# Kernel optimization log

Measured on AMD Instinct MI355X. Metric: run time of the kernel, lower is better.

## Reference

```python
import jax, jax.numpy as jnp
import numpy as np

B, D, N, M = 64, 128, 400, 50
H, KD = 8, 16
NCONV, K, PAD = 4, 7, 3
MAXTS = 10000.0


def _pe(l):
    # PositionEncoding: freqs/phases interleave sin/cos as sin(pos*f + phase)
    i = np.arange(D)
    freqs = MAXTS ** np.where(i % 2 == 0, -i / D, -(i - 1) / D)
    phases = np.where(i % 2 == 0, 0.0, np.pi / 2)
    pos = np.arange(l)
    return jnp.asarray(np.sin(pos[None, :] * freqs[:, None] + phases[:, None]).astype(np.float32))  # [D, l]


def _ln(x, g, b, eps=1e-6):
    # LayerNorm1d over channel dim of [B, D, L]; torch .std() is unbiased (ddof=1), divides by (std+eps)
    mu = x.mean(axis=1, keepdims=True)
    sd = x.std(axis=1, keepdims=True, ddof=1)
    return g[None, :, None] * (x - mu) / (sd + eps) + b[None, :, None]


def _attn(xT, mask, Wq, bq, Wk, bk, Wv, bv, Wo, bo):
    # xT: [B, L, D]; per-head linears vectorized over the head axis
    q = jnp.einsum('bld,hdk->bhlk', xT, Wq) + bq[None, :, None, :]
    k = jnp.einsum('bld,hdk->bhlk', xT, Wk) + bk[None, :, None, :]
    v = jnp.einsum('bld,hdk->bhlk', xT, Wv) + bv[None, :, None, :]
    sc = jnp.einsum('bhik,bhjk->bhij', q, k) / np.sqrt(KD)
    sc = sc - 1e30 * (1.0 - mask[:, None, None, :])  # mask over key positions
    a = jax.nn.softmax(sc, axis=-1)
    o = jnp.einsum('bhij,bhjk->bhik', a, v)
    o = o.transpose(0, 2, 1, 3).reshape(xT.shape[0], xT.shape[1], H * KD)
    return o @ Wo + bo


def _fwd(context_emb, question_emb, c_mask, q_mask, ln_g, ln_b, dw_w, dw_b, pw_w, pw_b,
         Wq, bq, Wk, bk, Wv, bv, Wo, bo, Wfc, bfc, cq_wc, cq_wq, cq_wm, cq_b):
    def block(x, mask):
        out = x + _pe(x.shape[2])[None]
        for i in range(NCONV):  # fixed small layer loop
            res = out
            h = _ln(out, ln_g, ln_b)
            h = jax.lax.conv_general_dilated(h, dw_w[i], (1,), [(PAD, PAD)],
                                             feature_group_count=D,
                                             dimension_numbers=('NCH', 'OIH', 'NCH')) + dw_b[i][None, :, None]
            h = jnp.einsum('bdl,ed->bel', h, pw_w[i]) + pw_b[i][None, :, None]
            out = jax.nn.relu(h) + res  # eval-mode layer_dropout = inputs + residual
        res = out
        h = _ln(out, ln_g, ln_b)
        h = _attn(h.transpose(0, 2, 1), mask, Wq, bq, Wk, bk, Wv, bv, Wo, bo)
        out = h.transpose(0, 2, 1) + res
        res = out
        h = _ln(out, ln_g, ln_b)
        h = jnp.einsum('bdl,ed->bel', h, Wfc) + bfc[None, :, None]
        return h + res

    C = block(context_emb, c_mask)
    Q = block(question_emb, q_mask)
    C2 = C.transpose(0, 2, 1)  # [B, N, D]
    Q2 = Q.transpose(0, 2, 1)  # [B, M, D]
    # Biaffine similarity W0([Q; C; Q*C]) decomposed (same math, no [B,N*M,3D] materialization)
    S = (C2 @ cq_wc)[:, :, None] + (Q2 @ cq_wq)[:, None, :] \
        + jnp.einsum('bnd,bmd->bnm', C2 * cq_wm, Q2) + cq_b[0]
    S_r = jax.nn.softmax(S - 1e30 * (1.0 - q_mask[:, None, :]), axis=2)
    S_c = jax.nn.softmax(S - 1e30 * (1.0 - c_mask[:, :, None]), axis=1)
    A = S_r @ Q2                                    # context-to-query [B, N, D]
    Bt = jnp.einsum('bnm,bkm->bnk', S_r, S_c) @ C2  # query-to-context (DCN style) [B, N, D]
    return jnp.concatenate([C2, A, C2 * A, C2 * Bt], axis=-1)  # [B, N, 4D]


def setup_inputs() -> dict:
    key = jax.random.key(0)
    ks = jax.random.split(key, 16)
    s = 1.0 / np.sqrt(D)
    return dict(
        context_emb=jax.random.normal(ks[0], (B, D, N), jnp.float32),
        question_emb=jax.random.normal(ks[1], (B, D, M), jnp.float32),
        c_mask=jnp.ones((B, N), jnp.float32),
        q_mask=jnp.ones((B, M), jnp.float32),
        ln_g=jnp.ones((D,), jnp.float32),
        ln_b=jnp.zeros((D,), jnp.float32),
        dw_w=jax.random.normal(ks[2], (NCONV, D, 1, K), jnp.float32) / np.sqrt(K),
        dw_b=jnp.zeros((NCONV, D), jnp.float32),
        pw_w=jax.random.normal(ks[3], (NCONV, D, D), jnp.float32) * s,
        pw_b=jnp.zeros((NCONV, D), jnp.float32),
        Wq=jax.random.normal(ks[4], (H, D, KD), jnp.float32) * s,
        bq=jnp.zeros((H, KD), jnp.float32),
        Wk=jax.random.normal(ks[5], (H, D, KD), jnp.float32) * s,
        bk=jnp.zeros((H, KD), jnp.float32),
        Wv=jax.random.normal(ks[6], (H, D, KD), jnp.float32) * s,
        bv=jnp.zeros((H, KD), jnp.float32),
        Wo=jax.random.normal(ks[7], (H * KD, D), jnp.float32) * s,
        bo=jnp.zeros((D,), jnp.float32),
        Wfc=jax.random.normal(ks[8], (D, D), jnp.float32) * s,
        bfc=jnp.zeros((D,), jnp.float32),
        cq_wc=jax.random.normal(ks[9], (D,), jnp.float32) * s,
        cq_wq=jax.random.normal(ks[10], (D,), jnp.float32) * s,
        cq_wm=jax.random.normal(ks[11], (D,), jnp.float32) * s,
        cq_b=jnp.zeros((1,), jnp.float32),
    )


def reference(context_emb, question_emb, c_mask, q_mask, ln_g, ln_b, dw_w, dw_b, pw_w, pw_b,
              Wq, bq, Wk, bk, Wv, bv, Wo, bo, Wfc, bfc, cq_wc, cq_wq, cq_wm, cq_b):
    return _fwd(context_emb, question_emb, c_mask, q_mask, ln_g, ln_b, dw_w, dw_b, pw_w, pw_b,
                Wq, bq, Wk, bk, Wv, bv, Wo, bo, Wfc, bfc, cq_wc, cq_wq, cq_wm, cq_b)
```

## Files before the change

### kernel.cpp

```cpp
#include <hip/hip_runtime.h>
#include <math.h>

#define BB 64
#define DD 128
#define NN 400
#define MM 50
#define HH 8
#define KDIM 16
#define NC 4
#define KW 7

#define SZ_C (BB * DD * NN)
#define SZ_Q (BB * DD * MM)
#define SSTAT (BB * NN + BB * MM)

__global__ void k_transposeW(const float* __restrict__ pw_w, const float* __restrict__ Wo,
                             const float* __restrict__ Wfc, const float* __restrict__ Wq,
                             const float* __restrict__ Wk, const float* __restrict__ Wv,
                             float* __restrict__ Wcan) {
  int idx = blockIdx.x * 256 + threadIdx.x;
  if (idx >= 9 * 16384) return;
  int m = idx >> 14;
  int r = idx & 16383;
  int d = r >> 7, e = r & 127;
  float v;
  if (m < 4) v = pw_w[m * 16384 + e * 128 + d];
  else if (m == 4) v = Wo[d * 128 + e];
  else if (m == 5) v = Wfc[e * 128 + d];
  else {
    const float* W = (m == 6) ? Wq : (m == 7) ? Wk : Wv;
    v = W[((e >> 4) * 128 + d) * 16 + (e & 15)];
  }
  Wcan[idx] = v;
}

__global__ void k_pestats(const float* __restrict__ xC, const float* __restrict__ xQ,
                          float* __restrict__ yC, float* __restrict__ yQ,
                          float* __restrict__ mu, float* __restrict__ inv) {
  int blk = blockIdx.x;
  const float* x; float* y; int L, l0, b, soff;
  if (blk < 448) { b = blk / 7; l0 = (blk % 7) * 64; x = xC; y = yC; L = NN; soff = 0; }
  else { b = blk - 448; l0 = 0; x = xQ; y = yQ; L = MM; soff = BB * NN; }
  int tid = threadIdx.x;
  int ll = tid & 63;
  int dq = tid >> 6;
  int l = l0 + ll;
  __shared__ float s_sum[4][64], s_sq[4][64];
  float sum = 0.f, sq = 0.f;
  if (l < L) {
    const float* px = x + (size_t)b * DD * L + l;
    float* py = y + (size_t)b * DD * L + l;
    for (int d = dq * 32; d < dq * 32 + 32; ++d) {
      int de = d & ~1;
      float freq = __expf((float)de * (-9.210340371976184f / 128.0f));
      float ph = (d & 1) ? 1.5707963267948966f : 0.0f;
      float v = px[(size_t)d * L] + sinf((float)l * freq + ph);
      py[(size_t)d * L] = v;
      sum += v; sq += v * v;
    }
  }
  s_sum[dq][ll] = sum; s_sq[dq][ll] = sq;
  __syncthreads();
  if (dq == 0 && l < L) {
    float ts = s_sum[0][ll] + s_sum[1][ll] + s_sum[2][ll] + s_sum[3][ll];
    float tq = s_sq[0][ll] + s_sq[1][ll] + s_sq[2][ll] + s_sq[3][ll];
    float m = ts * (1.0f / 128.0f);
    float var = (tq - 128.0f * m * m) * (1.0f / 127.0f);
    float sd = sqrtf(fmaxf(var, 0.f));
    mu[soff + b * L + l] = m;
    inv[soff + b * L + l] = 1.0f / (sd + 1e-6f);
  }
}

__global__ __launch_bounds__(256, 2) void k_convgemm(
    const float* __restrict__ xC, const float* __restrict__ xQ,
    float* __restrict__ outC, float* __restrict__ outQ,
    const float* __restrict__ Wc, const float* __restrict__ pwb,
    const float* __restrict__ dww, const float* __restrict__ dwb,
    const float* __restrict__ muI, const float* __restrict__ invI,
    float* __restrict__ muO, float* __restrict__ invO,
    const float* __restrict__ g, const float* __restrict__ beta) {
  int blk = blockIdx.x;
  int b = blk >> 3, tile = blk & 7;
  const float* x; float* out; int L, l0, soff;
  if (tile < 7) { x = xC; out = outC; L = NN; l0 = tile * 64; soff = 0; }
  else { x = xQ; out = outQ; L = MM; l0 = 0; soff = BB * NN; }
  __shared__ float Wl[32 * 128];
  __shared__ float Xl[32 * 64];
  __shared__ float Sm[70], Si[70];
  int tid = threadIdx.x;
  const float* xb = x + (size_t)b * DD * L;
  for (int t = tid; t < 70; t += 256) {
    int gl = l0 + t - 3;
    bool ok = (gl >= 0 && gl < L);
    Sm[t] = ok ? muI[soff + b * L + gl] : 0.f;
    Si[t] = ok ? invI[soff + b * L + gl] : 0.f;
  }
  float acc[8][4];
  #pragma unroll
  for (int i = 0; i < 8; ++i)
    #pragma unroll
    for (int j = 0; j < 4; ++j) acc[i][j] = 0.f;
  __syncthreads();
  for (int kc = 0; kc < 4; ++kc) {
    int d0 = kc * 32;
    #pragma unroll
    for (int i = 0; i < 4; ++i) {
      int idx = i * 256 + tid;
      ((float4*)Wl)[idx] = ((const float4*)Wc)[(size_t)d0 * 32 + idx];
    }
    #pragma unroll
    for (int r = 0; r < 2; ++r) {
      int k = r * 16 + (tid >> 4);
      int d = d0 + k;
      int c0 = (tid & 15) * 4;
      const float* xrow = xb + (size_t)d * L;
      float gd = g[d], bd = beta[d];
      float wv[7];
      #pragma unroll
      for (int u = 0; u < 7; ++u) wv[u] = dww[d * 7 + u];
      float dbv = dwb[d];
      float xw[10];
      int gbase = l0 + c0 - 3;
      if (gbase >= 1 && gbase + 11 <= L && (((unsigned)(d * L + gbase - 1)) & 3u) == 0u) {
        const float4* p = (const float4*)&xrow[gbase - 1];
        float4 A = p[0], Bv = p[1], Cv = p[2];
        float xr[12] = {A.x, A.y, A.z, A.w, Bv.x, Bv.y, Bv.z, Bv.w, Cv.x, Cv.y, Cv.z, Cv.w};
        #pragma unroll
        for (int s = 0; s < 10; ++s)
          xw[s] = gd * (xr[s + 1] - Sm[c0 + s]) * Si[c0 + s] + bd;
      } else {
        #pragma unroll
        for (int s = 0; s < 10; ++s) {
          int gl = gbase + s;
          float v = 0.f;
          if (gl >= 0 && gl < L)
            v = gd * (xrow[gl] - Sm[c0 + s]) * Si[c0 + s] + bd;
          xw[s] = v;
        }
      }
      float4 o;
      o.x = dbv; o.y = dbv; o.z = dbv; o.w = dbv;
      #pragma unroll
      for (int u = 0; u < 7; ++u) {
        o.x += wv[u] * xw[u];
        o.y += wv[u] * xw[u + 1];
        o.z += wv[u] * xw[u + 2];
        o.w += wv[u] * xw[u + 3];
      }
      *(float4*)&Xl[k * 64 + c0] = o;
    }
    __syncthreads();
    int e0 = (tid >> 4) * 8, cq = (tid & 15) * 4;
    for (int k = 0; k < 32; ++k) {
      const float4* wp = (const float4*)&Wl[k * 128 + e0];
      float4 w0 = wp[0], w1 = wp[1];
      float4 xv = *(const float4*)&Xl[k * 64 + cq];
      float we[8] = {w0.x, w0.y, w0.z, w0.w, w1.x, w1.y, w1.z, w1.w};
      float xe[4] = {xv.x, xv.y, xv.z, xv.w};
      #pragma unroll
      for (int i = 0; i < 8; ++i)
        #pragma unroll
        for (int j = 0; j < 4; ++j) acc[i][j] += we[i] * xe[j];
    }
    __syncthreads();
  }
  int e0 = (tid >> 4) * 8, cq = (tid & 15) * 4;
  float ssum[4], ssq[4];
  #pragma unroll
  for (int j = 0; j < 4; ++j) { ssum[j] = 0.f; ssq[j] = 0.f; }
  #pragma unroll
  for (int i = 0; i < 8; ++i) {
    float bi = pwb[e0 + i];
    float* po = out + ((size_t)b * DD + e0 + i) * L;
    const float* pr = xb + (size_t)(e0 + i) * L;
    #pragma unroll
    for (int j = 0; j < 4; ++j) {
      int l = l0 + cq + j;
      if (l < L) {
        float v = fmaxf(acc[i][j] + bi, 0.f) + pr[l];
        po[l] = v;
        ssum[j] += v; ssq[j] += v * v;
      }
    }
  }
  int grp = tid >> 4;
  #pragma unroll
  for (int j = 0; j < 4; ++j) {
    Xl[grp * 64 + cq + j] = ssum[j];
    Wl[grp * 64 + cq + j] = ssq[j];
  }
  __syncthreads();
  if (tid < 64) {
    int l = l0 + tid;
    if (l < L) {
      float ts = 0.f, tq = 0.f;
      #pragma unroll
      for (int gg = 0; gg < 16; ++gg) { ts += Xl[gg * 64 + tid]; tq += Wl[gg * 64 + tid]; }
      float m = ts * (1.0f / 128.0f);
      float var = (tq - 128.0f * m * m) * (1.0f / 127.0f);
      float sd = sqrtf(fmaxf(var, 0.f));
      muO[soff + b * L + l] = m;
      invO[soff + b * L + l] = 1.0f / (sd + 1e-6f);
    }
  }
}

template <int LNF, int ACT, int STATS>
__global__ __launch_bounds__(256) void k_gemm64(
    const float* __restrict__ xC, const float* __restrict__ xQ,
    float* __restrict__ outC, float* __restrict__ outQ,
    const float* __restrict__ Wc, const float* __restrict__ bias,
    const float* __restrict__ mu, const float* __restrict__ inv,
    float* __restrict__ muO, float* __restrict__ invO,
    const float* __restrict__ g, const float* __restrict__ beta) {
  int blk = blockIdx.x;
  int b = blk >> 3, tile = blk & 7;
  const float* x; float* out; int L, l0, soff;
  if (tile < 7) { x = xC; out = outC; L = NN; l0 = tile * 64; soff = 0; }
  else { x = xQ; out = outQ; L = MM; l0 = 0; soff = BB * NN; }
  __shared__ float Wl[32 * 128];
  __shared__ float Xl[32 * 64];
  int tid = threadIdx.x;
  float acc[8][4];
  #pragma unroll
  for (int i = 0; i < 8; ++i)
    #pragma unroll
    for (int j = 0; j < 4; ++j) acc[i][j] = 0.f;
  const float* xb = x + (size_t)b * DD * L;
  const float* pmu = mu + soff + b * L;
  const float* pin = inv + soff + b * L;
  for (int kc = 0; kc < 4; ++kc) {
    int d0 = kc * 32;
    #pragma unroll
    for (int i = 0; i < 4; ++i) {
      int idx = i * 256 + tid;
      ((float4*)Wl)[idx] = ((const float4*)Wc)[(size_t)d0 * 32 + idx];
    }
    #pragma unroll
    for (int t = 0; t < 8; ++t) {
      int idx = t * 256 + tid;
      int k = idx >> 6, l = idx & 63;
      float v = 0.f;
      int gl = l0 + l;
      if (gl < L) {
        v = xb[(size_t)(d0 + k) * L + gl];
        if (LNF) v = g[d0 + k] * (v - pmu[gl]) * pin[gl] + beta[d0 + k];
      }
      Xl[idx] = v;
    }
    __syncthreads();
    int e0 = (tid >> 4) * 8, cq = (tid & 15) * 4;
    for (int k = 0; k < 32; ++k) {
      const float4* wp = (const float4*)&Wl[k * 128 + e0];
      float4 w0 = wp[0], w1 = wp[1];
      float4 xv = *(const float4*)&Xl[k * 64 + cq];
      float we[8] = {w0.x, w0.y, w0.z, w0.w, w1.x, w1.y, w1.z, w1.w};
      float xe[4] = {xv.x, xv.y, xv.z, xv.w};
      #pragma unroll
      for (int i = 0; i < 8; ++i)
        #pragma unroll
        for (int j = 0; j < 4; ++j) acc[i][j] += we[i] * xe[j];
    }
    __syncthreads();
  }
  int e0 = (tid >> 4) * 8, cq = (tid & 15) * 4;
  float ssum[4], ssq[4];
  #pragma unroll
  for (int j = 0; j < 4; ++j) { ssum[j] = 0.f; ssq[j] = 0.f; }
  #pragma unroll
  for (int i = 0; i < 8; ++i) {
    float bi = bias[e0 + i];
    float* po = out + ((size_t)b * DD + e0 + i) * L;
    #pragma unroll
    for (int j = 0; j < 4; ++j) {
      int l = l0 + cq + j;
      if (l < L) {
        float v = acc[i][j] + bi;
        if (ACT != 0) v += po[l];
        po[l] = v;
        if (STATS) { ssum[j] += v; ssq[j] += v * v; }
      }
    }
  }
  if (STATS) {
    int grp = tid >> 4;
    #pragma unroll
    for (int j = 0; j < 4; ++j) {
      Xl[grp * 64 + cq + j] = ssum[j];
      Wl[grp * 64 + cq + j] = ssq[j];
    }
    __syncthreads();
    if (tid < 64) {
      int l = l0 + tid;
      if (l < L) {
        float ts = 0.f, tq = 0.f;
        #pragma unroll
        for (int gg = 0; gg < 16; ++gg) { ts += Xl[gg * 64 + tid]; tq += Wl[gg * 64 + tid]; }
        float m = ts * (1.0f / 128.0f);
        float var = (tq - 128.0f * m * m) * (1.0f / 127.0f);
        float sd = sqrtf(fmaxf(var, 0.f));
        muO[soff + b * L + l] = m;
        invO[soff + b * L + l] = 1.0f / (sd + 1e-6f);
      }
    }
  }
}

__global__ __launch_bounds__(256) void k_gemm_qkv(
    const float* __restrict__ xC, const float* __restrict__ xQ,
    float* __restrict__ o1C, float* __restrict__ o1Q,
    float* __restrict__ o2C, float* __restrict__ o2Q,
    float* __restrict__ o3C, float* __restrict__ o3Q,
    const float* __restrict__ Wcan,
    const float* __restrict__ bq, const float* __restrict__ bk, const float* __restrict__ bv,
    const float* __restrict__ mu, const float* __restrict__ inv,
    const float* __restrict__ g, const float* __restrict__ beta) {
  int blk0 = blockIdx.x;
  int grp = blk0 >> 9;
  int blk = blk0 & 511;
  const float* Wc = Wcan + (size_t)(6 + grp) * 16384;
  const float* bias = (grp == 0) ? bq : (grp == 1) ? bk : bv;
  float* oC = (grp == 0) ? o1C : (grp == 1) ? o2C : o3C;
  float* oQ = (grp == 0) ? o1Q : (grp == 1) ? o2Q : o3Q;
  int b = blk >> 3, tile = blk & 7;
  const float* x; float* out; int L, l0, soff;
  if (tile < 7) { x = xC; out = oC; L = NN; l0 = tile * 64; soff = 0; }
  else { x = xQ; out = oQ; L = MM; l0 = 0; soff = BB * NN; }
  __shared__ float Wl[32 * 128];
  __shared__ float Xl[32 * 64];
  int tid = threadIdx.x;
  float acc[8][4];
  #pragma unroll
  for (int i = 0; i < 8; ++i)
    #pragma unroll
    for (int j = 0; j < 4; ++j) acc[i][j] = 0.f;
  const float* xb = x + (size_t)b * DD * L;
  const float* pmu = mu + soff + b * L;
  const float* pin = inv + soff + b * L;
  for (int kc = 0; kc < 4; ++kc) {
    int d0 = kc * 32;
    #pragma unroll
    for (int i = 0; i < 4; ++i) {
      int idx = i * 256 + tid;
      ((float4*)Wl)[idx] = ((const float4*)Wc)[(size_t)d0 * 32 + idx];
    }
    #pragma unroll
    for (int t = 0; t < 8; ++t) {
      int idx = t * 256 + tid;
      int k = idx >> 6, l = idx & 63;
      float v = 0.f;
      int gl = l0 + l;
      if (gl < L) {
        v = xb[(size_t)(d0 + k) * L + gl];
        v = g[d0 + k] * (v - pmu[gl]) * pin[gl] + beta[d0 + k];
      }
      Xl[idx] = v;
    }
    __syncthreads();
    int e0 = (tid >> 4) * 8, cq = (tid & 15) * 4;
    for (int k = 0; k < 32; ++k) {
      const float4* wp = (const float4*)&Wl[k * 128 + e0];
      float4 w0 = wp[0], w1 = wp[1];
      float4 xv = *(const float4*)&Xl[k * 64 + cq];
      float we[8] = {w0.x, w0.y, w0.z, w0.w, w1.x, w1.y, w1.z, w1.w};
      float xe[4] = {xv.x, xv.y, xv.z, xv.w};
      #pragma unroll
      for (int i = 0; i < 8; ++i)
        #pragma unroll
        for (int j = 0; j < 4; ++j) acc[i][j] += we[i] * xe[j];
    }
    __syncthreads();
  }
  int e0 = (tid >> 4) * 8, cq = (tid & 15) * 4;
  #pragma unroll
  for (int i = 0; i < 8; ++i) {
    float bi = bias[e0 + i];
    float* po = out + ((size_t)b * DD + e0 + i) * L;
    #pragma unroll
    for (int j = 0; j < 4; ++j) {
      int l = l0 + cq + j;
      if (l < L) po[l] = acc[i][j] + bi;
    }
  }
}

__global__ __launch_bounds__(256) void k_attn2(
    const float* __restrict__ qC, const float* __restrict__ kC, const float* __restrict__ vC,
    const float* __restrict__ qQ, const float* __restrict__ kQ, const float* __restrict__ vQ,
    const float* __restrict__ cmask, const float* __restrict__ qmask,
    float* __restrict__ oC, float* __restrict__ oQ) {
  int blk = blockIdx.x;
  const float *qp, *kp, *vp, *mk; float* op; int L, b, h, q0, qcnt;
  if (blk < 1024) {
    b = blk >> 4; h = (blk >> 1) & 7; int half = blk & 1;
    qp = qC; kp = kC; vp = vC; mk = cmask; op = oC; L = NN;
    q0 = half * 256; qcnt = half ? (NN - 256) : 256;
  } else {
    int bb = blk - 1024; b = bb >> 3; h = bb & 7;
    qp = qQ; kp = kQ; vp = vQ; mk = qmask; op = oQ; L = MM;
    q0 = 0; qcnt = MM;
  }
  __shared__ float Kl[NN * KDIM];
  __shared__ float Vl[NN * KDIM];
  __shared__ float Ml[NN];
  int tid = threadIdx.x;
  size_t base = ((size_t)b * DD + h * KDIM) * L;
  int KP = (L + 7) & ~7;
  for (int idx = tid; idx < KDIM * L; idx += 256) {
    int t = idx / L, j = idx - t * L;
    Kl[j * KDIM + t] = kp[base + (size_t)t * L + j];
    Vl[j * KDIM + t] = vp[base + (size_t)t * L + j];
  }
  for (int idx = tid; idx < (KP - L) * KDIM; idx += 256) {
    int j = L + (idx >> 4), t = idx & 15;
    Kl[j * KDIM + t] = 0.f; Vl[j * KDIM + t] = 0.f;
  }
  for (int j = tid; j < KP; j += 256)
    Ml[j] = (j < L) ? -1e30f * (1.0f - mk[b * L + j]) : -1e30f;
  __syncthreads();
  if (tid >= qcnt) return;

  int i = q0 + tid;
  float q[KDIM];
  #pragma unroll
  for (int t = 0; t < KDIM; ++t) q[t] = qp[base + (size_t)t * L + i] * 0.25f;
  float m = -1e30f, ls = 0.f;
  float acc[KDIM];
  #pragma unroll
  for (int t = 0; t < KDIM; ++t) acc[t] = 0.f;
  for (int j0 = 0; j0 < KP; j0 += 8) {
    const float4* mp = (const float4*)&Ml[j0];
    float4 ma0 = mp[0], ma1 = mp[1];
    float mav[8] = {ma0.x, ma0.y, ma0.z, ma0.w, ma1.x, ma1.y, ma1.z, ma1.w};
    float s[8];
    #pragma unroll
    for (int jj = 0; jj < 8; ++jj) {
      const float4* kf = (const float4*)&Kl[(j0 + jj) * KDIM];
      float4 k0 = kf[0], k1 = kf[1], k2 = kf[2], k3 = kf[3];
      float da = q[0] * k0.x + q[1] * k0.y + q[2] * k0.z + q[3] * k0.w
               + q[4] * k1.x + q[5] * k1.y + q[6] * k1.z + q[7] * k1.w;
      float db = q[8] * k2.x + q[9] * k2.y + q[10] * k2.z + q[11] * k2.w
               + q[12] * k3.x + q[13] * k3.y + q[14] * k3.z + q[15] * k3.w;
      s[jj] = da + db + mav[jj];
    }
    float cm = s[0];
    #pragma unroll
    for (int jj = 1; jj < 8; ++jj) cm = fmaxf(cm, s[jj]);
    if (cm > m) {
      float sc = __expf(m - cm);
      ls *= sc;
      #pragma unroll
      for (int t = 0; t < KDIM; ++t) acc[t] *= sc;
      m = cm;
    }
    #pragma unroll
    for (int jj = 0; jj < 8; ++jj) {
      float p = __expf(s[jj] - m);
      ls += p;
      const float4* vf = (const float4*)&Vl[(j0 + jj) * KDIM];
      float4 v0 = vf[0], v1 = vf[1], v2 = vf[2], v3 = vf[3];
      acc[0] += p * v0.x;  acc[1] += p * v0.y;  acc[2] += p * v0.z;  acc[3] += p * v0.w;
      acc[4] += p * v1.x;  acc[5] += p * v1.y;  acc[6] += p * v1.z;  acc[7] += p * v1.w;
      acc[8] += p * v2.x;  acc[9] += p * v2.y;  acc[10] += p * v2.z; acc[11] += p * v2.w;
      acc[12] += p * v3.x; acc[13] += p * v3.y; acc[14] += p * v3.z; acc[15] += p * v3.w;
    }
  }
  float invl = 1.0f / ls;
  #pragma unroll
  for (int t = 0; t < KDIM; ++t)
    op[base + (size_t)t * L + i] = acc[t] * invl;
}

__global__ void k_prep(const float* __restrict__ Cb, const float* __restrict__ Qb,
                       float* __restrict__ C2, float* __restrict__ Q2,
                       const float* __restrict__ wc, const float* __restrict__ wq,
                       float* __restrict__ cd, float* __restrict__ qd) {
  int blk = blockIdx.x, tid = threadIdx.x;
  if (blk < 3840) {
    const float* X; float* Y; int L, rem;
    if (blk < 3328) { X = Cb; Y = C2; L = NN; rem = blk; }
    else { X = Qb; Y = Q2; L = MM; rem = blk - 3328; }
    int ntl = (L + 31) / 32;
    int b = rem / (4 * ntl);
    int r2 = rem % (4 * ntl);
    int d0 = (r2 / ntl) * 32;
    int l0 = (r2 % ntl) * 32;
    __shared__ float T[32][33];
    int c = tid & 31, r8 = tid >> 5;
    const float* xb = X + (size_t)b * DD * L;
    #pragma unroll
    for (int k = 0; k < 4; ++k) {
      int r = r8 + k * 8;
      int l = l0 + c;
      T[r][c] = (l < L) ? xb[(size_t)(d0 + r) * L + l] : 0.f;
    }
    __syncthreads();
    float* yb = Y + (size_t)b * L * DD;
    #pragma unroll
    for (int k = 0; k < 4; ++k) {
      int rr = r8 + k * 8;
      int l = l0 + rr;
      if (l < L) yb[(size_t)l * DD + d0 + c] = T[c][rr];
    }
  } else if (blk < 3940) {
    int idx = (blk - 3840) * 256 + tid;
    if (idx < BB * NN) {
      int l = idx % NN, b = idx / NN;
      const float* px = Cb + (size_t)b * DD * NN + l;
      float acc = 0.f;
      for (int d = 0; d < DD; ++d) acc += px[(size_t)d * NN] * wc[d];
      cd[idx] = acc;
    }
  } else {
    int idx = (blk - 3940) * 256 + tid;
    if (idx < BB * MM) {
      int l = idx % MM, b = idx / MM;
      const float* px = Qb + (size_t)b * DD * MM + l;
      float acc = 0.f;
      for (int d = 0; d < DD; ++d) acc += px[(size_t)d * MM] * wq[d];
      qd[idx] = acc;
    }
  }
}

__global__ void k_S(const float* __restrict__ C2, const float* __restrict__ Q2,
                    const float* __restrict__ cd, const float* __restrict__ qd,
                    const float* __restrict__ wm, const float* __restrict__ bias,
                    float* __restrict__ S) {
  int idx = blockIdx.x * 256 + threadIdx.x;
  if (idx >= BB * NN * MM) return;
  int mcol = idx % MM;
  int n = (idx / MM) % NN;
  int b = idx / (MM * NN);
  const float4* pc = (const float4*)(C2 + ((size_t)b * NN + n) * DD);
  const float4* pq = (const float4*)(Q2 + ((size_t)b * MM + mcol) * DD);
  const float4* pw = (const float4*)wm;
  float a0 = 0.f, a1 = 0.f;
  #pragma unroll 4
  for (int d4 = 0; d4 < 32; d4 += 2) {
    float4 c0 = pc[d4], w0 = pw[d4], q0 = pq[d4];
    float4 c1 = pc[d4 + 1], w1 = pw[d4 + 1], q1 = pq[d4 + 1];
    a0 += (c0.x * w0.x) * q0.x + (c0.y * w0.y) * q0.y + (c0.z * w0.z) * q0.z + (c0.w * w0.w) * q0.w;
    a1 += (c1.x * w1.x) * q1.x + (c1.y * w1.y) * q1.y + (c1.z * w1.z) * q1.z + (c1.w * w1.w) * q1.w;
  }
  S[idx] = a0 + a1 + cd[b * NN + n] + qd[b * MM + mcol] + bias[0];
}

__global__ void k_smax(const float* __restrict__ S, float* __restrict__ Sr,
                       float* __restrict__ Sc, const float* __restrict__ cmask,
                       const float* __restrict__ qmask) {
  int blk = blockIdx.x;
  int tid = threadIdx.x;
  if (blk < BB * MM) {
    int b = blk / MM;
    int mcol = blk % MM;
    float vals[7];
    float mx = -1e30f;
    #pragma unroll
    for (int c = 0; c < 7; ++c) {
      int n = tid + c * 64;
      float s = -1e30f;
      if (n < NN)
        s = S[((size_t)b * NN + n) * MM + mcol] - 1e30f * (1.0f - cmask[b * NN + n]);
      vals[c] = s;
      mx = fmaxf(mx, s);
    }
    #pragma unroll
    for (int off = 1; off < 64; off <<= 1) mx = fmaxf(mx, __shfl_xor(mx, off));
    float sum = 0.f;
    #pragma unroll
    for (int c = 0; c < 7; ++c) { vals[c] = __expf(vals[c] - mx); sum += vals[c]; }
    #pragma unroll
    for (int off = 1; off < 64; off <<= 1) sum += __shfl_xor(sum, off);
    float inv = 1.0f / sum;
    #pragma unroll
    for (int c = 0; c < 7; ++c) {
      int n = tid + c * 64;
      if (n < NN) Sc[((size_t)b * NN + n) * MM + mcol] = vals[c] * inv;
    }
  } else {
    int bn = blk - BB * MM;
    int b = bn / NN;
    float s = -1e30f;
    if (tid < MM)
      s = S[(size_t)bn * MM + tid] - 1e30f * (1.0f - qmask[b * MM + tid]);
    float mx = s;
    #pragma unroll
    for (int off = 1; off < 64; off <<= 1) mx = fmaxf(mx, __shfl_xor(mx, off));
    float e = (tid < MM) ? __expf(s - mx) : 0.f;
    float sum = e;
    #pragma unroll
    for (int off = 1; off < 64; off <<= 1) sum += __shfl_xor(sum, off);
    if (tid < MM) Sr[(size_t)bn * MM + tid] = e / sum;
  }
}

__global__ void k_U(const float* __restrict__ Sc, const float* __restrict__ C2,
                    float* __restrict__ U) {
  int idx = blockIdx.x * 256 + threadIdx.x;
  if (idx >= BB * MM * 32) return;
  int d4 = idx & 31;
  int rest = idx >> 5;
  int mcol = rest % MM;
  int b = rest / MM;
  const float* psc = Sc + (size_t)b * NN * MM + mcol;
  const float4* pc2 = (const float4*)(C2 + (size_t)b * NN * DD) + d4;
  float4 acc = {0.f, 0.f, 0.f, 0.f};
  #pragma unroll 4
  for (int kk = 0; kk < NN; ++kk) {
    float s = psc[(size_t)kk * MM];
    float4 c = pc2[(size_t)kk * 32];
    acc.x += s * c.x; acc.y += s * c.y; acc.z += s * c.z; acc.w += s * c.w;
  }
  ((float4*)U)[idx] = acc;
}

__global__ __launch_bounds__(256) void k_ABtF(
    const float* __restrict__ Sr, const float* __restrict__ Q2,
    const float* __restrict__ Uu, const float* __restrict__ C2,
    float* __restrict__ out) {
  int blk = blockIdx.x;
  int b = blk / 7, nt = blk % 7;
  int n0 = nt * 64;
  int nv = NN - n0; if (nv > 64) nv = 64;
  __shared__ float Ql[MM * 128];
  __shared__ float Ul[MM * 128];
  __shared__ float Sl[64 * MM];
  int tid = threadIdx.x;
  const float4* q4 = (const float4*)(Q2 + (size_t)b * MM * DD);
  const float4* u4 = (const float4*)(Uu + (size_t)b * MM * DD);
  for (int i = tid; i < MM * 32; i += 256) {
    ((float4*)Ql)[i] = q4[i];
    ((float4*)Ul)[i] = u4[i];
  }
  for (int i = tid; i < 64 * MM; i += 256) {
    int n = i / MM;
    Sl[i] = (n < nv) ? Sr[((size_t)b * NN + n0 + n) * MM + (i - n * MM)] : 0.f;
  }
  __syncthreads();
  int n = tid >> 2;
  if (n >= nv) return;
  int d04 = (tid & 3) * 8;
  float4 accA[8], accB[8];
  #pragma unroll
  for (int r = 0; r < 8; ++r) {
    accA[r] = {0.f, 0.f, 0.f, 0.f};
    accB[r] = {0.f, 0.f, 0.f, 0.f};
  }
  const float* sp = &Sl[n * MM];
  for (int m = 0; m < MM; ++m) {
    float s = sp[m];
    const float4* qp = (const float4*)&Ql[m * 128] + d04;
    const float4* up = (const float4*)&Ul[m * 128] + d04;
    #pragma unroll
    for (int r = 0; r < 8; ++r) {
      float4 q = qp[r], u = up[r];
      accA[r].x += s * q.x; accA[r].y += s * q.y; accA[r].z += s * q.z; accA[r].w += s * q.w;
      accB[r].x += s * u.x; accB[r].y += s * u.y; accB[r].z += s * u.z; accB[r].w += s * u.w;
    }
  }
  int gn = n0 + n;
  const float4* c4 = (const float4*)(C2 + ((size_t)b * NN + gn) * DD) + d04;
  float4* po = (float4*)(out + (size_t)(b * NN + gn) * 512);
  #pragma unroll
  for (int r = 0; r < 8; ++r) {
    float4 c = c4[r];
    float4 a = accA[r], bt = accB[r];
    po[d04 + r] = c;
    po[32 + d04 + r] = a;
    float4 ca = {c.x * a.x, c.y * a.y, c.z * a.z, c.w * a.w};
    po[64 + d04 + r] = ca;
    float4 cb = {c.x * bt.x, c.y * bt.y, c.z * bt.z, c.w * bt.w};
    po[96 + d04 + r] = cb;
  }
}

extern "C" void kernel_launch(void* const* d_in, const int* in_sizes, int n_in,
                              void* d_out, int out_size, void* d_ws, size_t ws_size,
                              hipStream_t stream) {
  (void)in_sizes; (void)n_in; (void)out_size; (void)ws_size;
  const float* ctx   = (const float*)d_in[0];
  const float* que   = (const float*)d_in[1];
  const float* cmask = (const float*)d_in[2];
  const float* qmask = (const float*)d_in[3];
  const float* ln_g  = (const float*)d_in[4];
  const float* ln_b  = (const float*)d_in[5];
  const float* dw_w  = (const float*)d_in[6];
  const float* dw_b  = (const float*)d_in[7];
  const float* pw_w  = (const float*)d_in[8];
  const float* pw_b  = (const float*)d_in[9];
  const float* Wq    = (const float*)d_in[10];
  const float* bq    = (const float*)d_in[11];
  const float* Wk    = (const float*)d_in[12];
  const float* bk    = (const float*)d_in[13];
  const float* Wv    = (const float*)d_in[14];
  const float* bv    = (const float*)d_in[15];
  const float* Wo    = (const float*)d_in[16];
  const float* bo    = (const float*)d_in[17];
  const float* Wfc   = (const float*)d_in[18];
  const float* bfc   = (const float*)d_in[19];
  const float* cq_wc = (const float*)d_in[20];
  const float* cq_wq = (const float*)d_in[21];
  const float* cq_wm = (const float*)d_in[22];
  const float* cq_b  = (const float*)d_in[23];
  float* out = (float*)d_out;
  float* ws = (float*)d_ws;

  float* Cb   = ws;
  float* Qb   = Cb + SZ_C;
  float* t1C  = Qb + SZ_Q;
  float* t1Q  = t1C + SZ_C;
  float* t2C  = t1Q + SZ_Q;
  float* t2Q  = t2C + SZ_C;
  float* t3C  = t2Q + SZ_Q;
  float* t3Q  = t3C + SZ_C;
  float* t4C  = t3Q + SZ_Q;
  float* t4Q  = t4C + SZ_C;
  float* mu0  = t4Q + SZ_Q;
  float* inv0 = mu0 + SSTAT;
  float* mu1  = inv0 + SSTAT;
  float* inv1 = mu1 + SSTAT;
  float* Wcan = inv1 + SSTAT;

  k_transposeW<<<(9 * 16384 + 255) / 256, 256, 0, stream>>>(pw_w, Wo, Wfc, Wq, Wk, Wv, Wcan);
  k_pestats<<<512, 256, 0, stream>>>(ctx, que, Cb, Qb, mu0, inv0);

  for (int i = 0; i < NC; ++i) {
    const float* inC = (i & 1) ? t1C : Cb;
    const float* inQ = (i & 1) ? t1Q : Qb;
    float* oC = (i & 1) ? Cb : t1C;
    float* oQ = (i & 1) ? Qb : t1Q;
    const float* mI = (i & 1) ? mu1 : mu0;
    const float* iI = (i & 1) ? inv1 : inv0;
    float* mO = (i & 1) ? mu0 : mu1;
    float* iO = (i & 1) ? inv0 : inv1;
    k_convgemm<<<512, 256, 0, stream>>>(inC, inQ, oC, oQ,
                                        Wcan + (size_t)i * 16384, pw_b + (size_t)i * DD,
                                        dw_w + (size_t)i * DD * KW, dw_b + (size_t)i * DD,
                                        mI, iI, mO, iO, ln_g, ln_b);
  }
  k_gemm_qkv<<<1536, 256, 0, stream>>>(Cb, Qb, t1C, t1Q, t2C, t2Q, t3C, t3Q,
                                       Wcan, bq, bk, bv, mu0, inv0, ln_g, ln_b);
  k_attn2<<<1536, 256, 0, stream>>>(t1C, t2C, t3C, t1Q, t2Q, t3Q, cmask, qmask, t4C, t4Q);
  k_gemm64<0, 1, 1><<<512, 256, 0, stream>>>(t4C, t4Q, Cb, Qb, Wcan + 4 * 16384, bo,
                                             mu0, inv0, mu1, inv1, ln_g, ln_b);
  k_gemm64<1, 1, 0><<<512, 256, 0, stream>>>(Cb, Qb, Cb, Qb, Wcan + 5 * 16384, bfc,
                                             mu1, inv1, mu0, inv0, ln_g, ln_b);

  float* C2  = t1C;
  float* Q2  = t1Q;
  float* S   = t2C;
  float* Sr  = t2C + 1638400;
  float* Scb = t3C;
  float* Uu  = t2Q;
  float* cd  = t3Q;
  float* qd  = t4Q;

  k_prep<<<3953, 256, 0, stream>>>(Cb, Qb, C2, Q2, cq_wc, cq_wq, cd, qd);
  k_S<<<(BB * NN * MM + 255) / 256, 256, 0, stream>>>(C2, Q2, cd, qd, cq_wm, cq_b, S);
  k_smax<<<BB * MM + BB * NN, 64, 0, stream>>>(S, Sr, Scb, cmask, qmask);
  k_U<<<(BB * MM * 32 + 255) / 256, 256, 0, stream>>>(Scb, C2, Uu);
  k_ABtF<<<448, 256, 0, stream>>>(Sr, Q2, Uu, C2, out);
}
```

Before: 721.5 us.

## Tile trilinear similarity kernel through shared memory with register blocking

Replaces the one-thread-per-output similarity kernel with a tiled version. Each block stages 64 context rows (pre-scaled by the weight vector) and all 50 question rows of one batch in LDS. Each thread then computes 13 outputs from registers, so every global element is read once per block instead of once per output. This trades a large amount of redundant global/L2 traffic for about 60KB of LDS per block, which limits occupancy, and some padded work on the last tile.

```diff
diff --git a/kernel.cpp b/kernel.cpp
--- a/kernel.cpp
+++ b/kernel.cpp
@@ -524,27 +524,65 @@
   }
 }
 
-__global__ void k_S(const float* __restrict__ C2, const float* __restrict__ Q2,
-                    const float* __restrict__ cd, const float* __restrict__ qd,
-                    const float* __restrict__ wm, const float* __restrict__ bias,
-                    float* __restrict__ S) {
-  int idx = blockIdx.x * 256 + threadIdx.x;
-  if (idx >= BB * NN * MM) return;
-  int mcol = idx % MM;
-  int n = (idx / MM) % NN;
-  int b = idx / (MM * NN);
-  const float4* pc = (const float4*)(C2 + ((size_t)b * NN + n) * DD);
-  const float4* pq = (const float4*)(Q2 + ((size_t)b * MM + mcol) * DD);
-  const float4* pw = (const float4*)wm;
-  float a0 = 0.f, a1 = 0.f;
-  #pragma unroll 4
-  for (int d4 = 0; d4 < 32; d4 += 2) {
-    float4 c0 = pc[d4], w0 = pw[d4], q0 = pq[d4];
-    float4 c1 = pc[d4 + 1], w1 = pw[d4 + 1], q1 = pq[d4 + 1];
-    a0 += (c0.x * w0.x) * q0.x + (c0.y * w0.y) * q0.y + (c0.z * w0.z) * q0.z + (c0.w * w0.w) * q0.w;
-    a1 += (c1.x * w1.x) * q1.x + (c1.y * w1.y) * q1.y + (c1.z * w1.z) * q1.z + (c1.w * w1.w) * q1.w;
-  }
-  S[idx] = a0 + a1 + cd[b * NN + n] + qd[b * MM + mcol] + bias[0];
+__global__ __launch_bounds__(256) void k_S2(
+    const float* __restrict__ C2, const float* __restrict__ Q2,
+    const float* __restrict__ cd, const float* __restrict__ qd,
+    const float* __restrict__ wm, const float* __restrict__ bias,
+    float* __restrict__ S) {
+  int blk = blockIdx.x;
+  int b = blk / 7, nt = blk % 7;
+  int n0 = nt * 64;
+  int nv = NN - n0; if (nv > 64) nv = 64;
+  __shared__ float Cw[64 * 132];
+  __shared__ float Ql[52 * 132];
+  __shared__ float cdl[64];
+  __shared__ float qdl[50];
+  int tid = threadIdx.x;
+  const float4* c4g = (const float4*)(C2 + (size_t)b * NN * DD);
+  const float4* q4g = (const float4*)(Q2 + (size_t)b * MM * DD);
+  const float4* w4 = (const float4*)wm;
+  for (int i = tid; i < 64 * 32; i += 256) {
+    int n = i >> 5, d4 = i & 31;
+    float4 v = {0.f, 0.f, 0.f, 0.f};
+    if (n < nv) {
+      float4 c = c4g[(size_t)(n0 + n) * 32 + d4];
+      float4 w = w4[d4];
+      v.x = c.x * w.x; v.y = c.y * w.y; v.z = c.z * w.z; v.w = c.w * w.w;
+    }
+    *(float4*)&Cw[n * 132 + d4 * 4] = v;
+  }
+  for (int i = tid; i < 52 * 32; i += 256) {
+    int m = i >> 5, d4 = i & 31;
+    float4 v = {0.f, 0.f, 0.f, 0.f};
+    if (m < MM) v = q4g[(size_t)m * 32 + d4];
+    *(float4*)&Ql[m * 132 + d4 * 4] = v;
+  }
+  if (tid < 64) cdl[tid] = (tid < nv) ? cd[b * NN + n0 + tid] : 0.f;
+  if (tid >= 64 && tid < 114) qdl[tid - 64] = qd[b * MM + (tid - 64)];
+  __syncthreads();
+  int n = tid >> 2, mg = tid & 3;
+  int m0 = mg * 13;
+  float acc[13];
+  #pragma unroll
+  for (int k = 0; k < 13; ++k) acc[k] = 0.f;
+  const float* cp = &Cw[n * 132];
+  for (int d4 = 0; d4 < 32; ++d4) {
+    float4 c = *(const float4*)&cp[d4 * 4];
+    #pragma unroll
+    for (int k = 0; k < 13; ++k) {
+      float4 q = *(const float4*)&Ql[(m0 + k) * 132 + d4 * 4];
+      acc[k] += c.x * q.x + c.y * q.y + c.z * q.z + c.w * q.w;
+    }
+  }
+  if (n < nv) {
+    float add = cdl[n] + bias[0];
+    float* ps = S + ((size_t)b * NN + n0 + n) * MM + m0;
+    #pragma unroll
+    for (int k = 0; k < 13; ++k) {
+      int m = m0 + k;
+      if (m < MM) ps[k] = acc[k] + add + qdl[m];
+    }
+  }
 }
 
 __global__ void k_smax(const float* __restrict__ S, float* __restrict__ Sr,
@@ -758,7 +796,7 @@
   float* qd  = t4Q;
 
   k_prep<<<3953, 256, 0, stream>>>(Cb, Qb, C2, Q2, cq_wc, cq_wq, cd, qd);
-  k_S<<<(BB * NN * MM + 255) / 256, 256, 0, stream>>>(C2, Q2, cd, qd, cq_wm, cq_b, S);
+  k_S2<<<448, 256, 0, stream>>>(C2, Q2, cd, qd, cq_wm, cq_b, S);
   k_smax<<<BB * MM + BB * NN, 64, 0, stream>>>(S, Sr, Scb, cmask, qmask);
   k_U<<<(BB * MM * 32 + 255) / 256, 256, 0, stream>>>(Scb, C2, Uu);
   k_ABtF<<<448, 256, 0, stream>>>(Sr, Q2, Uu, C2, out);
```

Measured after the change: 644.2 us. 10.7% less time.
